# Kernel tuning notes

Measured on AMD Instinct MI355X. Metric: run time of the kernel, lower is better.

## Reference

```python
import jax, jax.numpy as jnp
import numpy as np

D = 1024
H = 16
L = 2048
B = 2
EPS = 1e-5


def setup_inputs() -> dict:
    key = jax.random.key(0)
    ks = jax.random.split(key, 12)
    s = 0.02
    return {
        "x": jax.random.normal(ks[0], (B, L, D), dtype=jnp.float32),
        "ln1_w": jnp.ones((D,), jnp.float32),
        "ln1_b": jnp.zeros((D,), jnp.float32),
        "ln2_w": jnp.ones((D,), jnp.float32),
        "ln2_b": jnp.zeros((D,), jnp.float32),
        "attn_w": jax.random.normal(ks[1], (D, 3 * D), jnp.float32) * s,
        "attn_b": jnp.zeros((3 * D,), jnp.float32),
        "proj_w": jax.random.normal(ks[2], (D, D), jnp.float32) * s,
        "proj_b": jnp.zeros((D,), jnp.float32),
        "fc1_w": jax.random.normal(ks[3], (D, 4 * D), jnp.float32) * s,
        "fc1_b": jnp.zeros((4 * D,), jnp.float32),
        "fc2_w": jax.random.normal(ks[4], (4 * D, D), jnp.float32) * s,
        "fc2_b": jnp.zeros((D,), jnp.float32),
    }


def layernorm(x, w, b):
    mu = jnp.mean(x, axis=-1, keepdims=True)
    var = jnp.mean(jnp.square(x - mu), axis=-1, keepdims=True)
    return (x - mu) * jax.lax.rsqrt(var + EPS) * w + b


def reference(x, ln1_w, ln1_b, ln2_w, ln2_b, attn_w, attn_b,
              proj_w, proj_b, fc1_w, fc1_b, fc2_w, fc2_b):
    Bsz, Lq, C = x.shape
    hd = C // H

    # --- attention branch ---
    h = layernorm(x, ln1_w, ln1_b)
    qkv = h @ attn_w + attn_b                      # [B, L, 3C]
    q, k, v = jnp.split(qkv, 3, axis=-1)
    q = q.reshape(Bsz, Lq, H, hd).transpose(0, 2, 1, 3)  # [B, H, L, hd]
    k = k.reshape(Bsz, Lq, H, hd).transpose(0, 2, 1, 3)
    v = v.reshape(Bsz, Lq, H, hd).transpose(0, 2, 1, 3)

    # NOTE: original scales by 1/sqrt(embedding_dim), not sqrt(head_dim)
    att = jnp.einsum('bhqd,bhkd->bhqk', q, k) / jnp.sqrt(jnp.float32(C))
    causal = jnp.tril(jnp.ones((Lq, Lq), dtype=bool))
    att = jnp.where(causal[None, None], att, jnp.float32(-jnp.inf))
    att = jax.nn.softmax(att, axis=-1)
    y = jnp.einsum('bhqk,bhkd->bhqd', att, v)      # [B, H, L, hd]
    y = y.transpose(0, 2, 1, 3).reshape(Bsz, Lq, C)
    y = y @ proj_w + proj_b
    x = x + y

    # --- MLP branch ---
    h = layernorm(x, ln2_w, ln2_b)
    h = jax.nn.gelu(h @ fc1_w + fc1_b, approximate=False)
    h = h @ fc2_w + fc2_b
    return x + h
```

## Files before the change

### kernel.cpp

```cpp
#include <hip/hip_runtime.h>

#define Bsz 2
#define Lq  2048
#define Dm  1024
#define Hh  16

typedef __attribute__((ext_vector_type(8))) short bf16x8;
typedef __attribute__((ext_vector_type(4))) float f32x4;

#define MFMA16(a, b, c) __builtin_amdgcn_mfma_f32_16x16x32_bf16((a), (b), (c), 0, 0, 0)
#define EXP2F(x) __builtin_amdgcn_exp2f(x)

__device__ __forceinline__ short f2bf(float f) {
    union { float f; unsigned u; } v; v.f = f;
    unsigned r = v.u + 0x7fffu + ((v.u >> 16) & 1u);
    return (short)(r >> 16);
}

__device__ __forceinline__ float bf2f(unsigned short s) {
    union { float f; unsigned u; } t; t.u = ((unsigned)s) << 16;
    return t.f;
}

__device__ __forceinline__ int pk2(float a, float b) {
    union { float f; unsigned u; } ua, ub; ua.f = a; ub.f = b;
    return (int)((ua.u >> 16) | (ub.u & 0xffff0000u));
}

__device__ __forceinline__ void gload16(const void* g, void* l) {
    __builtin_amdgcn_global_load_lds((const __attribute__((address_space(1))) void*)g,
                                     (__attribute__((address_space(3))) void*)l,
                                     16, 0, 0);
}

__global__ __launch_bounds__(256) void ln_bf16(const float* __restrict__ x,
                                               const float* __restrict__ w,
                                               const float* __restrict__ b,
                                               short* __restrict__ out) {
    const int row = blockIdx.x;
    const int tid = threadIdx.x;
    const float4 v = ((const float4*)(x + (size_t)row * 1024))[tid];
    float s = v.x + v.y + v.z + v.w;
    float q = v.x * v.x + v.y * v.y + v.z * v.z + v.w * v.w;
    for (int off = 32; off > 0; off >>= 1) {
        s += __shfl_down(s, off);
        q += __shfl_down(q, off);
    }
    __shared__ float red[8];
    const int wave = tid >> 6;
    if ((tid & 63) == 0) { red[wave] = s; red[wave + 4] = q; }
    __syncthreads();
    s = red[0] + red[1] + red[2] + red[3];
    q = red[4] + red[5] + red[6] + red[7];
    const float mu = s * (1.0f / 1024.0f);
    const float var = q * (1.0f / 1024.0f) - mu * mu;
    const float rstd = rsqrtf(var + 1e-5f);
    const float4 wv = ((const float4*)w)[tid];
    const float4 bv = ((const float4*)b)[tid];
    short4 o;
    o.x = f2bf((v.x - mu) * rstd * wv.x + bv.x);
    o.y = f2bf((v.y - mu) * rstd * wv.y + bv.y);
    o.z = f2bf((v.z - mu) * rstd * wv.z + bv.z);
    o.w = f2bf((v.w - mu) * rstd * wv.w + bv.w);
    ((short4*)(out + (size_t)row * 1024))[tid] = o;
}

__global__ __launch_bounds__(256) void tr_cvt_all(
    const float* __restrict__ attnw, const float* __restrict__ projw,
    const float* __restrict__ fc1w,  const float* __restrict__ fc2w,
    short* __restrict__ attnwT, short* __restrict__ projwT,
    short* __restrict__ fc1wT,  short* __restrict__ fc2wT) {
    int id = blockIdx.x;
    const float* W; short* Wt; int K, N, bx, by;
    if (id < 3072)      { W = attnw; Wt = attnwT; K = 1024; N = 3072; bx = id % 96;  by = id / 96; }
    else if (id < 4096) { id -= 3072; W = projw; Wt = projwT; K = 1024; N = 1024; bx = id & 31; by = id >> 5; }
    else if (id < 8192) { id -= 4096; W = fc1w;  Wt = fc1wT;  K = 1024; N = 4096; bx = id & 127; by = id >> 7; }
    else                { id -= 8192; W = fc2w;  Wt = fc2wT;  K = 4096; N = 1024; bx = id & 31; by = id >> 5; }
    __shared__ float t[32][33];
    const int n0 = bx * 32, k0 = by * 32;
    const int tx = threadIdx.x & 31, ty = threadIdx.x >> 5;
#pragma unroll
    for (int i = 0; i < 4; i++)
        t[ty + i * 8][tx] = W[(size_t)(k0 + ty + i * 8) * N + n0 + tx];
    __syncthreads();
#pragma unroll
    for (int i = 0; i < 4; i++)
        Wt[(size_t)(n0 + ty + i * 8) * K + k0 + tx] = f2bf(t[tx][ty + i * 8]);
}

template <int EP>
__global__ __launch_bounds__(256, 4) void gemm_bt(
    const short* __restrict__ A, const short* __restrict__ Bt,
    const float* __restrict__ bias, int N, int K,
    short* __restrict__ qd, short* __restrict__ kd, short* __restrict__ vtd,
    short* __restrict__ outb) {
    __shared__ short As[128 * 32];
    __shared__ short Bs[128 * 32];
    const int tid = threadIdx.x;
    const int lane = tid & 63, w = tid >> 6;
    const int l16 = lane & 15, quad = lane >> 4;
    const int wr = (w & 1) * 64, wc = (w >> 1) * 64;
    const int n = blockIdx.x;
    const int row0 = ((n & 7) * 4 + ((n >> 3) & 3)) * 128;
    const int col0 = (n >> 5) * 128;
    const int srow = lane >> 2, scol = (lane & 3) * 8;

    f32x4 acc[4][4];
    const f32x4 z = {0.f, 0.f, 0.f, 0.f};
#pragma unroll
    for (int i = 0; i < 4; i++)
#pragma unroll
        for (int j = 0; j < 4; j++) acc[i][j] = z;

    const size_t arow = (size_t)(row0 + w * 32 + srow);
    const size_t brow = (size_t)(col0 + w * 32 + srow);

    for (int k0 = 0; k0 < K; k0 += 32) {
        gload16(A + arow * K + k0 + scol,        &As[(w * 32) * 32]);
        gload16(A + (arow + 16) * K + k0 + scol, &As[(w * 32 + 16) * 32]);
        gload16(Bt + brow * K + k0 + scol,        &Bs[(w * 32) * 32]);
        gload16(Bt + (brow + 16) * K + k0 + scol, &Bs[(w * 32 + 16) * 32]);
        __syncthreads();
        bf16x8 a[4], bb[4];
#pragma unroll
        for (int i = 0; i < 4; i++) a[i] = *(const bf16x8*)&As[(wr + i * 16 + l16) * 32 + quad * 8];
#pragma unroll
        for (int j = 0; j < 4; j++) bb[j] = *(const bf16x8*)&Bs[(wc + j * 16 + l16) * 32 + quad * 8];
#pragma unroll
        for (int i = 0; i < 4; i++)
#pragma unroll
            for (int j = 0; j < 4; j++) acc[i][j] = MFMA16(a[i], bb[j], acc[i][j]);
        __syncthreads();
    }

    float bz[4];
#pragma unroll
    for (int j = 0; j < 4; j++) bz[j] = bias[col0 + wc + j * 16 + l16];

#pragma unroll
    for (int i = 0; i < 4; i++) {
#pragma unroll
        for (int r = 0; r < 4; r++) {
            const int grow = row0 + wr + i * 16 + quad * 4 + r;
#pragma unroll
            for (int j = 0; j < 4; j++) {
                const int gcol = col0 + wc + j * 16 + l16;
                const float v = acc[i][j][r] + bz[j];
                if constexpr (EP == 0) {
                    const int b = grow >> 11, l = grow & 2047;
                    const int sec = gcol >> 10, wi = gcol & 1023;
                    const int h = wi >> 6, d = wi & 63;
                    if (sec == 2) {
                        vtd[(((size_t)b * Hh + h) * 64 + d) * Lq + l] = f2bf(v);
                    } else {
                        short* dst = sec ? kd : qd;
                        dst[(((size_t)b * Hh + h) * Lq + l) * 64 + d] = f2bf(v);
                    }
                } else {
                    const float g = 0.5f * v * (1.0f + erff(v * 0.70710678118f));
                    outb[(size_t)grow * N + gcol] = f2bf(g);
                }
            }
        }
    }
}

__global__ __launch_bounds__(256, 4) void gemm_sk(
    const short* __restrict__ A, const short* __restrict__ Bt, int K, int zbits,
    short* __restrict__ Cp) {
    __shared__ short As[128 * 32];
    __shared__ short Bs[128 * 32];
    const int tid = threadIdx.x;
    const int lane = tid & 63, w = tid >> 6;
    const int l16 = lane & 15, quad = lane >> 4;
    const int wr = (w & 1) * 64, wc = (w >> 1) * 64;
    const int n = blockIdx.x;
    const int xcd = n & 7, t = n >> 3;
    const int col = t & 7, u = t >> 3;
    const int c = xcd * (4 << zbits) + u;
    const int zsl = c & ((1 << zbits) - 1);
    const int row0 = (c >> zbits) * 128, col0 = col * 128;
    const int KS = K >> zbits;
    const int kbeg = zsl * KS, kend = kbeg + KS;
    const int srow = lane >> 2, scol = (lane & 3) * 8;

    f32x4 acc[4][4];
    const f32x4 z = {0.f, 0.f, 0.f, 0.f};
#pragma unroll
    for (int i = 0; i < 4; i++)
#pragma unroll
        for (int j = 0; j < 4; j++) acc[i][j] = z;

    const size_t arow = (size_t)(row0 + w * 32 + srow);
    const size_t brow = (size_t)(col0 + w * 32 + srow);

    for (int k0 = kbeg; k0 < kend; k0 += 32) {
        gload16(A + arow * K + k0 + scol,        &As[(w * 32) * 32]);
        gload16(A + (arow + 16) * K + k0 + scol, &As[(w * 32 + 16) * 32]);
        gload16(Bt + brow * K + k0 + scol,        &Bs[(w * 32) * 32]);
        gload16(Bt + (brow + 16) * K + k0 + scol, &Bs[(w * 32 + 16) * 32]);
        __syncthreads();
        bf16x8 a[4], bb[4];
#pragma unroll
        for (int i = 0; i < 4; i++) a[i] = *(const bf16x8*)&As[(wr + i * 16 + l16) * 32 + quad * 8];
#pragma unroll
        for (int j = 0; j < 4; j++) bb[j] = *(const bf16x8*)&Bs[(wc + j * 16 + l16) * 32 + quad * 8];
#pragma unroll
        for (int i = 0; i < 4; i++)
#pragma unroll
            for (int j = 0; j < 4; j++) acc[i][j] = MFMA16(a[i], bb[j], acc[i][j]);
        __syncthreads();
    }

    short* cp = Cp + (size_t)zsl * 4096 * 1024;
#pragma unroll
    for (int i = 0; i < 4; i++) {
#pragma unroll
        for (int r = 0; r < 4; r++) {
            const int grow = row0 + wr + i * 16 + quad * 4 + r;
#pragma unroll
            for (int j = 0; j < 4; j++) {
                const int gcol = col0 + wc + j * 16 + l16;
                cp[(size_t)grow * 1024 + gcol] = f2bf(acc[i][j][r]);
            }
        }
    }
}

__global__ __launch_bounds__(256) void sk_reduce(const short* __restrict__ Cp, int S,
                                                 const float* __restrict__ res,
                                                 const float* __restrict__ bias,
                                                 float* __restrict__ out) {
    const int row = blockIdx.x, tid = threadIdx.x;
    const size_t base = (size_t)row * 1024 + tid * 4;
    float4 a = ((const float4*)(res + (size_t)row * 1024))[tid];
    const float4 bz = ((const float4*)bias)[tid];
    a.x += bz.x; a.y += bz.y; a.z += bz.z; a.w += bz.w;
    for (int s = 0; s < S; s++) {
        const ushort4 c = *(const ushort4*)(Cp + (size_t)s * 4096 * 1024 + base);
        a.x += bf2f(c.x); a.y += bf2f(c.y); a.z += bf2f(c.z); a.w += bf2f(c.w);
    }
    *(float4*)(out + base) = a;
}

__global__ __launch_bounds__(256) void sk_reduce_ln(const short* __restrict__ Cp, int S,
                                                    const float* __restrict__ res,
                                                    const float* __restrict__ bias,
                                                    const float* __restrict__ lnw,
                                                    const float* __restrict__ lnb,
                                                    float* __restrict__ xout,
                                                    short* __restrict__ hout) {
    const int row = blockIdx.x, tid = threadIdx.x;
    const size_t base = (size_t)row * 1024 + tid * 4;
    float4 a = ((const float4*)(res + (size_t)row * 1024))[tid];
    const float4 bz = ((const float4*)bias)[tid];
    a.x += bz.x; a.y += bz.y; a.z += bz.z; a.w += bz.w;
    for (int s = 0; s < S; s++) {
        const ushort4 c = *(const ushort4*)(Cp + (size_t)s * 4096 * 1024 + base);
        a.x += bf2f(c.x); a.y += bf2f(c.y); a.z += bf2f(c.z); a.w += bf2f(c.w);
    }
    *(float4*)(xout + base) = a;
    float sm = a.x + a.y + a.z + a.w;
    float qs = a.x * a.x + a.y * a.y + a.z * a.z + a.w * a.w;
    for (int off = 32; off > 0; off >>= 1) {
        sm += __shfl_down(sm, off);
        qs += __shfl_down(qs, off);
    }
    __shared__ float red[8];
    const int wave = tid >> 6;
    if ((tid & 63) == 0) { red[wave] = sm; red[wave + 4] = qs; }
    __syncthreads();
    sm = red[0] + red[1] + red[2] + red[3];
    qs = red[4] + red[5] + red[6] + red[7];
    const float mu = sm * (1.0f / 1024.0f);
    const float var = qs * (1.0f / 1024.0f) - mu * mu;
    const float rstd = rsqrtf(var + 1e-5f);
    const float4 wv = ((const float4*)lnw)[tid];
    const float4 bv = ((const float4*)lnb)[tid];
    short4 o;
    o.x = f2bf((a.x - mu) * rstd * wv.x + bv.x);
    o.y = f2bf((a.y - mu) * rstd * wv.y + bv.y);
    o.z = f2bf((a.z - mu) * rstd * wv.z + bv.z);
    o.w = f2bf((a.w - mu) * rstd * wv.w + bv.w);
    ((short4*)(hout + (size_t)row * 1024))[tid] = o;
}

#define KP 72
__global__ __launch_bounds__(256, 2) void attn_kernel(const short* __restrict__ Q,
                                                      const short* __restrict__ Kb,
                                                      const short* __restrict__ Vt,
                                                      short* __restrict__ Y) {
    const int tid = threadIdx.x;
    const int lane = tid & 63, wave = tid >> 6;
    const int l16 = lane & 15, quad = lane >> 4;
    const int qblk = 15 - blockIdx.x;
    const int bh = blockIdx.y;
    const int qw = qblk * 128 + wave * 32;

    const short* qg = Q + ((size_t)bh * Lq + qw) * 64;
    const short* kg = Kb + (size_t)bh * Lq * 64;
    const short* vg = Vt + (size_t)bh * 64 * Lq;

    __shared__ short sKa[2][64 * 32], sKb[2][64 * 32];
    __shared__ short sVa[2][64 * 32], sVb[2][64 * 32];
    __shared__ short sP[4][32 * KP];
    short* wpP = sP[wave];

    const float c1 = 0.0450842213f;

    bf16x8 qf[2][2];
#pragma unroll
    for (int c = 0; c < 2; c++)
#pragma unroll
        for (int d = 0; d < 2; d++) {
            bf16x8 v = *(const bf16x8*)(qg + (c * 16 + l16) * 64 + d * 32 + quad * 8);
            bf16x8 r;
#pragma unroll
            for (int i = 0; i < 8; i++) {
                union { float f; unsigned u; } t;
                t.u = ((unsigned)(unsigned short)v[i]) << 16;
                r[i] = f2bf(t.f * c1);
            }
            qf[c][d] = r;
        }

    f32x4 o[4][2];
    const f32x4 z = {0.f, 0.f, 0.f, 0.f};
#pragma unroll
    for (int j = 0; j < 4; j++)
#pragma unroll
        for (int c = 0; c < 2; c++) o[j][c] = z;
    float l_i[2] = {0.f, 0.f};

    const int srow = wave * 16 + (lane >> 2);
    const int scol = (lane & 3) * 8;
    const int nst = 2 * qblk + 2;

    auto stage = [&](int s) {
        const int p = s & 1;
        const int kb = s * 64;
        gload16(kg + (size_t)(kb + srow) * 64 + scol,      &sKa[p][(wave * 16) * 32]);
        gload16(kg + (size_t)(kb + srow) * 64 + 32 + scol, &sKb[p][(wave * 16) * 32]);
        gload16(vg + (size_t)srow * Lq + kb + scol,        &sVa[p][(wave * 16) * 32]);
        gload16(vg + (size_t)srow * Lq + kb + 32 + scol,   &sVb[p][(wave * 16) * 32]);
    };

    stage(0);

    for (int s = 0; s < nst; ++s) {
        const int p = s & 1;
        __syncthreads();
        bf16x8 kf[4][2];
#pragma unroll
        for (int kt = 0; kt < 4; kt++) {
            kf[kt][0] = *(const bf16x8*)&sKa[p][(kt * 16 + l16) * 32 + quad * 8];
            kf[kt][1] = *(const bf16x8*)&sKb[p][(kt * 16 + l16) * 32 + quad * 8];
        }
        if (s + 1 < nst) stage(s + 1);

        f32x4 st[4][2];
#pragma unroll
        for (int kt = 0; kt < 4; kt++)
#pragma unroll
            for (int c = 0; c < 2; c++) {
                st[kt][c] = MFMA16(kf[kt][0], qf[c][0], z);
                st[kt][c] = MFMA16(kf[kt][1], qf[c][1], st[kt][c]);
            }

        const int rel = s * 64 - qblk * 128 - wave * 32;
        if (rel > -64) {
#pragma unroll
            for (int kt = 0; kt < 4; kt++)
#pragma unroll
                for (int c = 0; c < 2; c++)
#pragma unroll
                    for (int r = 0; r < 4; r++) {
                        const int krel = rel + kt * 16 + quad * 4 + r - c * 16;
                        if (krel > l16) st[kt][c][r] = -1e30f;
                    }
        }

#pragma unroll
        for (int c = 0; c < 2; c++) {
            float pv[4][4], rs = 0.f;
#pragma unroll
            for (int kt = 0; kt < 4; kt++)
#pragma unroll
                for (int r = 0; r < 4; r++) {
                    pv[kt][r] = EXP2F(st[kt][c][r]);
                    rs += pv[kt][r];
                }
            l_i[c] += rs;
            short* wp = wpP + (c * 16 + l16) * KP;
#pragma unroll
            for (int kt = 0; kt < 4; kt++) {
                int2 pw; pw.x = pk2(pv[kt][0], pv[kt][1]); pw.y = pk2(pv[kt][2], pv[kt][3]);
                *(int2*)(wp + kt * 16 + quad * 4) = pw;
            }
        }

        bf16x8 pf[2][2];
#pragma unroll
        for (int c = 0; c < 2; c++) {
            pf[c][0] = *(const bf16x8*)(wpP + (c * 16 + l16) * KP + quad * 8);
            pf[c][1] = *(const bf16x8*)(wpP + (c * 16 + l16) * KP + 32 + quad * 8);
        }
#pragma unroll
        for (int j = 0; j < 4; j++) {
            const bf16x8 v0 = *(const bf16x8*)&sVa[p][(j * 16 + l16) * 32 + quad * 8];
            const bf16x8 v1 = *(const bf16x8*)&sVb[p][(j * 16 + l16) * 32 + quad * 8];
#pragma unroll
            for (int c = 0; c < 2; c++) {
                o[j][c] = MFMA16(v0, pf[c][0], o[j][c]);
                o[j][c] = MFMA16(v1, pf[c][1], o[j][c]);
            }
        }
    }

    const int b = bh >> 4, h = bh & 15;
#pragma unroll
    for (int c = 0; c < 2; c++) {
        float ls = l_i[c];
        ls += __shfl_xor(ls, 16);
        ls += __shfl_xor(ls, 32);
        const float inv = 1.0f / ls;
        const size_t base = ((size_t)b * Lq + qw + c * 16 + l16) * 1024 + h * 64;
#pragma unroll
        for (int j = 0; j < 4; j++) {
            short4 s4;
            s4.x = f2bf(o[j][c][0] * inv);
            s4.y = f2bf(o[j][c][1] * inv);
            s4.z = f2bf(o[j][c][2] * inv);
            s4.w = f2bf(o[j][c][3] * inv);
            *(short4*)(Y + base + j * 16 + quad * 4) = s4;
        }
    }
}

extern "C" void kernel_launch(void* const* d_in, const int* in_sizes, int n_in,
                              void* d_out, int out_size, void* d_ws, size_t ws_size,
                              hipStream_t stream) {
    (void)in_sizes; (void)n_in; (void)out_size; (void)ws_size;
    const float* x     = (const float*)d_in[0];
    const float* ln1w  = (const float*)d_in[1];
    const float* ln1b  = (const float*)d_in[2];
    const float* ln2w  = (const float*)d_in[3];
    const float* ln2b  = (const float*)d_in[4];
    const float* attnw = (const float*)d_in[5];
    const float* attnb = (const float*)d_in[6];
    const float* projw = (const float*)d_in[7];
    const float* projb = (const float*)d_in[8];
    const float* fc1w  = (const float*)d_in[9];
    const float* fc1b  = (const float*)d_in[10];
    const float* fc2w  = (const float*)d_in[11];
    const float* fc2b  = (const float*)d_in[12];
    float* out = (float*)d_out;

    char* ws = (char*)d_ws;
    size_t off = 0;
    auto alloc = [&](size_t bytes) {
        void* p = ws + off;
        off += (bytes + 255) & ~(size_t)255;
        return p;
    };
    short* attnwT = (short*)alloc(3072ull * 1024 * 2);
    short* projwT = (short*)alloc(1024ull * 1024 * 2);
    short* fc1wT  = (short*)alloc(4096ull * 1024 * 2);
    short* fc2wT  = (short*)alloc(1024ull * 4096 * 2);
    short* hbuf   = (short*)alloc(4096ull * 1024 * 2);
    short* qbuf   = (short*)alloc(4096ull * 1024 * 2);
    short* kbuf   = (short*)alloc(4096ull * 1024 * 2);
    short* vtbuf  = (short*)alloc(4096ull * 1024 * 2);
    short* ybuf   = (short*)alloc(4096ull * 1024 * 2);
    float* x1     = (float*)alloc(4096ull * 1024 * 4);
    short* Cp     = (short*)alloc(4ull * 4096 * 1024 * 2);
    short* hh = qbuf;

    tr_cvt_all<<<12288, 256, 0, stream>>>(attnw, projw, fc1w, fc2w,
                                          attnwT, projwT, fc1wT, fc2wT);

    ln_bf16<<<4096, 256, 0, stream>>>(x, ln1w, ln1b, hbuf);
    gemm_bt<0><<<768, 256, 0, stream>>>(hbuf, attnwT, attnb, 3072, 1024,
                                        qbuf, kbuf, vtbuf, nullptr);
    attn_kernel<<<dim3(16, 32), 256, 0, stream>>>(qbuf, kbuf, vtbuf, ybuf);
    gemm_sk<<<512, 256, 0, stream>>>(ybuf, projwT, 1024, 1, Cp);
    sk_reduce_ln<<<4096, 256, 0, stream>>>(Cp, 2, x, projb, ln2w, ln2b, x1, hbuf);

    gemm_bt<2><<<1024, 256, 0, stream>>>(hbuf, fc1wT, fc1b, 4096, 1024,
                                         nullptr, nullptr, nullptr, hh);
    gemm_sk<<<1024, 256, 0, stream>>>(hh, fc2wT, 4096, 2, Cp);
    sk_reduce<<<4096, 256, 0, stream>>>(Cp, 4, x1, fc2b, out);
}
```

Baseline: 341.9 us.

## Replace GEMMs with 256x256-tile, 4-stage pipelined, LDS-swizzled kernel

```diff
diff --git a/kernel.cpp b/kernel.cpp
--- a/kernel.cpp
+++ b/kernel.cpp
@@ -89,64 +89,105 @@
 }
 
 template <int EP>
-__global__ __launch_bounds__(256, 4) void gemm_bt(
+__global__ __launch_bounds__(512, 2) void gemm256(
     const short* __restrict__ A, const short* __restrict__ Bt,
-    const float* __restrict__ bias, int N, int K,
+    const float* __restrict__ bias, int N, int K, int zbits,
     short* __restrict__ qd, short* __restrict__ kd, short* __restrict__ vtd,
     short* __restrict__ outb) {
-    __shared__ short As[128 * 32];
-    __shared__ short Bs[128 * 32];
+    __shared__ short sA[4][8192];
+    __shared__ short sB[4][8192];
     const int tid = threadIdx.x;
     const int lane = tid & 63, w = tid >> 6;
     const int l16 = lane & 15, quad = lane >> 4;
-    const int wr = (w & 1) * 64, wc = (w >> 1) * 64;
-    const int n = blockIdx.x;
-    const int row0 = ((n & 7) * 4 + ((n >> 3) & 3)) * 128;
-    const int col0 = (n >> 5) * 128;
-    const int srow = lane >> 2, scol = (lane & 3) * 8;
-
-    f32x4 acc[4][4];
+    const int wm = w >> 2, wn = w & 3;
+
+    const int wg = (blockIdx.x & 7) * ((int)gridDim.x >> 3) + ((int)blockIdx.x >> 3);
+    const int bm = wg & 15, rest = wg >> 4;
+    int bn, zsl = 0, kbase = 0, klen = K;
+    if constexpr (EP == 3) {
+        bn = rest & 3; zsl = rest >> 2;
+        klen = K >> zbits; kbase = zsl * klen;
+    } else {
+        bn = rest;
+    }
+    const int row0 = bm << 8, col0 = bn << 8;
+    const int NT = klen >> 5;
+
+    const int srow = w * 16 + (lane >> 2);
+    const int sslot = (lane & 3) ^ ((lane >> 2) & 3) ^ (lane >> 4);
+    const short* gA = A + (size_t)(row0 + srow) * K + kbase + sslot * 8;
+    const short* gB = Bt + (size_t)(col0 + srow) * K + kbase + sslot * 8;
+    const size_t rstr = (size_t)128 * K;
+
+    auto stage = [&](int t) {
+        const int p = t & 3;
+        const int ko = t << 5;
+        short* la = &sA[p][(w * 16) * 32];
+        short* lb = &sB[p][(w * 16) * 32];
+        gload16(gA + ko, la);
+        gload16(gA + rstr + ko, la + 4096);
+        gload16(gB + ko, lb);
+        gload16(gB + rstr + ko, lb + 4096);
+    };
+
+    f32x4 acc[8][4];
     const f32x4 z = {0.f, 0.f, 0.f, 0.f};
 #pragma unroll
-    for (int i = 0; i < 4; i++)
-#pragma unroll
-        for (int j = 0; j < 4; j++) acc[i][j] = z;
-
-    const size_t arow = (size_t)(row0 + w * 32 + srow);
-    const size_t brow = (size_t)(col0 + w * 32 + srow);
-
-    for (int k0 = 0; k0 < K; k0 += 32) {
-        gload16(A + arow * K + k0 + scol,        &As[(w * 32) * 32]);
-        gload16(A + (arow + 16) * K + k0 + scol, &As[(w * 32 + 16) * 32]);
-        gload16(Bt + brow * K + k0 + scol,        &Bs[(w * 32) * 32]);
-        gload16(Bt + (brow + 16) * K + k0 + scol, &Bs[(w * 32 + 16) * 32]);
-        __syncthreads();
-        bf16x8 a[4], bb[4];
-#pragma unroll
-        for (int i = 0; i < 4; i++) a[i] = *(const bf16x8*)&As[(wr + i * 16 + l16) * 32 + quad * 8];
-#pragma unroll
-        for (int j = 0; j < 4; j++) bb[j] = *(const bf16x8*)&Bs[(wc + j * 16 + l16) * 32 + quad * 8];
-#pragma unroll
-        for (int i = 0; i < 4; i++)
-#pragma unroll
-            for (int j = 0; j < 4; j++) acc[i][j] = MFMA16(a[i], bb[j], acc[i][j]);
-        __syncthreads();
+    for (int m = 0; m < 8; m++)
+#pragma unroll
+        for (int j = 0; j < 4; j++) acc[m][j] = z;
+
+    stage(0); stage(1); stage(2);
+
+    const int rslot = quad ^ (l16 & 3) ^ (l16 >> 2);
+    const int aoff = (wm * 128 + l16) * 32 + rslot * 8;
+    const int boff = (wn * 64 + l16) * 32 + rslot * 8;
+
+    for (int t = 0; t < NT; ++t) {
+        if (t + 3 < NT) stage(t + 3);
+        const int rem = NT - 1 - t;
+        if (rem >= 3)      asm volatile("s_waitcnt vmcnt(12)" ::: "memory");
+        else if (rem == 2) asm volatile("s_waitcnt vmcnt(8)" ::: "memory");
+        else if (rem == 1) asm volatile("s_waitcnt vmcnt(4)" ::: "memory");
+        else               asm volatile("s_waitcnt vmcnt(0)" ::: "memory");
+        __builtin_amdgcn_s_barrier();
+        __builtin_amdgcn_sched_barrier(0);
+        const int p = t & 3;
+        bf16x8 af[8], bf[4];
+#pragma unroll
+        for (int m = 0; m < 8; m++) af[m] = *(const bf16x8*)&sA[p][aoff + m * 512];
+#pragma unroll
+        for (int j = 0; j < 4; j++) bf[j] = *(const bf16x8*)&sB[p][boff + j * 512];
+        __builtin_amdgcn_s_setprio(1);
+#pragma unroll
+        for (int m = 0; m < 8; m++)
+#pragma unroll
+            for (int j = 0; j < 4; j++) acc[m][j] = MFMA16(af[m], bf[j], acc[m][j]);
+        __builtin_amdgcn_s_setprio(0);
+        asm volatile("s_waitcnt lgkmcnt(0)" ::: "memory");
+        __builtin_amdgcn_sched_barrier(0);
+        __builtin_amdgcn_s_barrier();
+        __builtin_amdgcn_sched_barrier(0);
     }
 
     float bz[4];
-#pragma unroll
-    for (int j = 0; j < 4; j++) bz[j] = bias[col0 + wc + j * 16 + l16];
-
-#pragma unroll
-    for (int i = 0; i < 4; i++) {
+    if constexpr (EP != 3) {
+#pragma unroll
+        for (int j = 0; j < 4; j++) bz[j] = bias[col0 + wn * 64 + j * 16 + l16];
+    }
+    short* cp = nullptr;
+    if constexpr (EP == 3) cp = outb + (size_t)zsl * 4096 * 1024;
+
+#pragma unroll
+    for (int m = 0; m < 8; m++) {
 #pragma unroll
         for (int r = 0; r < 4; r++) {
-            const int grow = row0 + wr + i * 16 + quad * 4 + r;
+            const int grow = row0 + wm * 128 + m * 16 + quad * 4 + r;
 #pragma unroll
             for (int j = 0; j < 4; j++) {
-                const int gcol = col0 + wc + j * 16 + l16;
-                const float v = acc[i][j][r] + bz[j];
+                const int gcol = col0 + wn * 64 + j * 16 + l16;
                 if constexpr (EP == 0) {
+                    const float v = acc[m][j][r] + bz[j];
                     const int b = grow >> 11, l = grow & 2047;
                     const int sec = gcol >> 10, wi = gcol & 1023;
                     const int h = wi >> 6, d = wi & 63;
@@ -156,72 +197,13 @@
                         short* dst = sec ? kd : qd;
                         dst[(((size_t)b * Hh + h) * Lq + l) * 64 + d] = f2bf(v);
                     }
-                } else {
+                } else if constexpr (EP == 2) {
+                    const float v = acc[m][j][r] + bz[j];
                     const float g = 0.5f * v * (1.0f + erff(v * 0.70710678118f));
                     outb[(size_t)grow * N + gcol] = f2bf(g);
+                } else {
+                    cp[(size_t)grow * 1024 + gcol] = f2bf(acc[m][j][r]);
                 }
-            }
-        }
-    }
-}
-
-__global__ __launch_bounds__(256, 4) void gemm_sk(
-    const short* __restrict__ A, const short* __restrict__ Bt, int K, int zbits,
-    short* __restrict__ Cp) {
-    __shared__ short As[128 * 32];
-    __shared__ short Bs[128 * 32];
-    const int tid = threadIdx.x;
-    const int lane = tid & 63, w = tid >> 6;
-    const int l16 = lane & 15, quad = lane >> 4;
-    const int wr = (w & 1) * 64, wc = (w >> 1) * 64;
-    const int n = blockIdx.x;
-    const int xcd = n & 7, t = n >> 3;
-    const int col = t & 7, u = t >> 3;
-    const int c = xcd * (4 << zbits) + u;
-    const int zsl = c & ((1 << zbits) - 1);
-    const int row0 = (c >> zbits) * 128, col0 = col * 128;
-    const int KS = K >> zbits;
-    const int kbeg = zsl * KS, kend = kbeg + KS;
-    const int srow = lane >> 2, scol = (lane & 3) * 8;
-
-    f32x4 acc[4][4];
-    const f32x4 z = {0.f, 0.f, 0.f, 0.f};
-#pragma unroll
-    for (int i = 0; i < 4; i++)
-#pragma unroll
-        for (int j = 0; j < 4; j++) acc[i][j] = z;
-
-    const size_t arow = (size_t)(row0 + w * 32 + srow);
-    const size_t brow = (size_t)(col0 + w * 32 + srow);
-
-    for (int k0 = kbeg; k0 < kend; k0 += 32) {
-        gload16(A + arow * K + k0 + scol,        &As[(w * 32) * 32]);
-        gload16(A + (arow + 16) * K + k0 + scol, &As[(w * 32 + 16) * 32]);
-        gload16(Bt + brow * K + k0 + scol,        &Bs[(w * 32) * 32]);
-        gload16(Bt + (brow + 16) * K + k0 + scol, &Bs[(w * 32 + 16) * 32]);
-        __syncthreads();
-        bf16x8 a[4], bb[4];
-#pragma unroll
-        for (int i = 0; i < 4; i++) a[i] = *(const bf16x8*)&As[(wr + i * 16 + l16) * 32 + quad * 8];
-#pragma unroll
-        for (int j = 0; j < 4; j++) bb[j] = *(const bf16x8*)&Bs[(wc + j * 16 + l16) * 32 + quad * 8];
-#pragma unroll
-        for (int i = 0; i < 4; i++)
-#pragma unroll
-            for (int j = 0; j < 4; j++) acc[i][j] = MFMA16(a[i], bb[j], acc[i][j]);
-        __syncthreads();
-    }
-
-    short* cp = Cp + (size_t)zsl * 4096 * 1024;
-#pragma unroll
-    for (int i = 0; i < 4; i++) {
-#pragma unroll
-        for (int r = 0; r < 4; r++) {
-            const int grow = row0 + wr + i * 16 + quad * 4 + r;
-#pragma unroll
-            for (int j = 0; j < 4; j++) {
-                const int gcol = col0 + wc + j * 16 + l16;
-                cp[(size_t)grow * 1024 + gcol] = f2bf(acc[i][j][r]);
             }
         }
     }
@@ -480,14 +462,16 @@
                                           attnwT, projwT, fc1wT, fc2wT);
 
     ln_bf16<<<4096, 256, 0, stream>>>(x, ln1w, ln1b, hbuf);
-    gemm_bt<0><<<768, 256, 0, stream>>>(hbuf, attnwT, attnb, 3072, 1024,
+    gemm256<0><<<192, 512, 0, stream>>>(hbuf, attnwT, attnb, 3072, 1024, 0,
                                         qbuf, kbuf, vtbuf, nullptr);
     attn_kernel<<<dim3(16, 32), 256, 0, stream>>>(qbuf, kbuf, vtbuf, ybuf);
-    gemm_sk<<<512, 256, 0, stream>>>(ybuf, projwT, 1024, 1, Cp);
+    gemm256<3><<<128, 512, 0, stream>>>(ybuf, projwT, nullptr, 1024, 1024, 1,
+                                        nullptr, nullptr, nullptr, Cp);
     sk_reduce_ln<<<4096, 256, 0, stream>>>(Cp, 2, x, projb, ln2w, ln2b, x1, hbuf);
 
-    gemm_bt<2><<<1024, 256, 0, stream>>>(hbuf, fc1wT, fc1b, 4096, 1024,
-                                         nullptr, nullptr, nullptr, hh);
-    gemm_sk<<<1024, 256, 0, stream>>>(hh, fc2wT, 4096, 2, Cp);
+    gemm256<2><<<256, 512, 0, stream>>>(hbuf, fc1wT, fc1b, 4096, 1024, 0,
+                                        nullptr, nullptr, nullptr, hh);
+    gemm256<3><<<256, 512, 0, stream>>>(hh, fc2wT, nullptr, 1024, 4096, 2,
+                                        nullptr, nullptr, nullptr, Cp);
     sk_reduce<<<4096, 256, 0, stream>>>(Cp, 4, x1, fc2b, out);
 }
```

New measurement: 407.2 us. 1.19x slower.

## Double GEMM K-tile to 64 with XOR-swizzled shared-memory layout

Applied to the files above, without the earlier changes.

```diff
diff --git a/kernel.cpp b/kernel.cpp
--- a/kernel.cpp
+++ b/kernel.cpp
@@ -94,8 +94,8 @@
     const float* __restrict__ bias, int N, int K,
     short* __restrict__ qd, short* __restrict__ kd, short* __restrict__ vtd,
     short* __restrict__ outb) {
-    __shared__ short As[128 * 32];
-    __shared__ short Bs[128 * 32];
+    __shared__ short As[128 * 64];
+    __shared__ short Bs[128 * 64];
     const int tid = threadIdx.x;
     const int lane = tid & 63, w = tid >> 6;
     const int l16 = lane & 15, quad = lane >> 4;
@@ -103,7 +103,8 @@
     const int n = blockIdx.x;
     const int row0 = ((n & 7) * 4 + ((n >> 3) & 3)) * 128;
     const int col0 = (n >> 5) * 128;
-    const int srow = lane >> 2, scol = (lane & 3) * 8;
+    const int srow = lane >> 3;
+    const int scol = ((lane & 7) ^ srow) * 8;
 
     f32x4 acc[4][4];
     const f32x4 z = {0.f, 0.f, 0.f, 0.f};
@@ -115,21 +116,26 @@
     const size_t arow = (size_t)(row0 + w * 32 + srow);
     const size_t brow = (size_t)(col0 + w * 32 + srow);
 
-    for (int k0 = 0; k0 < K; k0 += 32) {
-        gload16(A + arow * K + k0 + scol,        &As[(w * 32) * 32]);
-        gload16(A + (arow + 16) * K + k0 + scol, &As[(w * 32 + 16) * 32]);
-        gload16(Bt + brow * K + k0 + scol,        &Bs[(w * 32) * 32]);
-        gload16(Bt + (brow + 16) * K + k0 + scol, &Bs[(w * 32 + 16) * 32]);
+    for (int k0 = 0; k0 < K; k0 += 64) {
+#pragma unroll
+        for (int g = 0; g < 4; g++) {
+            gload16(A + (arow + g * 8) * K + k0 + scol,  &As[(w * 32 + g * 8) * 64]);
+            gload16(Bt + (brow + g * 8) * K + k0 + scol, &Bs[(w * 32 + g * 8) * 64]);
+        }
         __syncthreads();
-        bf16x8 a[4], bb[4];
-#pragma unroll
-        for (int i = 0; i < 4; i++) a[i] = *(const bf16x8*)&As[(wr + i * 16 + l16) * 32 + quad * 8];
-#pragma unroll
-        for (int j = 0; j < 4; j++) bb[j] = *(const bf16x8*)&Bs[(wc + j * 16 + l16) * 32 + quad * 8];
-#pragma unroll
-        for (int i = 0; i < 4; i++)
-#pragma unroll
-            for (int j = 0; j < 4; j++) acc[i][j] = MFMA16(a[i], bb[j], acc[i][j]);
+#pragma unroll
+        for (int kk = 0; kk < 2; kk++) {
+            const int rsl = ((kk * 4 + quad) ^ (l16 & 7)) * 8;
+            bf16x8 a[4], bb[4];
+#pragma unroll
+            for (int i = 0; i < 4; i++) a[i] = *(const bf16x8*)&As[(wr + i * 16 + l16) * 64 + rsl];
+#pragma unroll
+            for (int j = 0; j < 4; j++) bb[j] = *(const bf16x8*)&Bs[(wc + j * 16 + l16) * 64 + rsl];
+#pragma unroll
+            for (int i = 0; i < 4; i++)
+#pragma unroll
+                for (int j = 0; j < 4; j++) acc[i][j] = MFMA16(a[i], bb[j], acc[i][j]);
+        }
         __syncthreads();
     }
 
@@ -168,8 +174,8 @@
 __global__ __launch_bounds__(256, 4) void gemm_sk(
     const short* __restrict__ A, const short* __restrict__ Bt, int K, int zbits,
     short* __restrict__ Cp) {
-    __shared__ short As[128 * 32];
-    __shared__ short Bs[128 * 32];
+    __shared__ short As[128 * 64];
+    __shared__ short Bs[128 * 64];
     const int tid = threadIdx.x;
     const int lane = tid & 63, w = tid >> 6;
     const int l16 = lane & 15, quad = lane >> 4;
@@ -182,7 +188,8 @@
     const int row0 = (c >> zbits) * 128, col0 = col * 128;
     const int KS = K >> zbits;
     const int kbeg = zsl * KS, kend = kbeg + KS;
-    const int srow = lane >> 2, scol = (lane & 3) * 8;
+    const int srow = lane >> 3;
+    const int scol = ((lane & 7) ^ srow) * 8;
 
     f32x4 acc[4][4];
     const f32x4 z = {0.f, 0.f, 0.f, 0.f};
@@ -194,21 +201,26 @@
     const size_t arow = (size_t)(row0 + w * 32 + srow);
     const size_t brow = (size_t)(col0 + w * 32 + srow);
 
-    for (int k0 = kbeg; k0 < kend; k0 += 32) {
-        gload16(A + arow * K + k0 + scol,        &As[(w * 32) * 32]);
-        gload16(A + (arow + 16) * K + k0 + scol, &As[(w * 32 + 16) * 32]);
-        gload16(Bt + brow * K + k0 + scol,        &Bs[(w * 32) * 32]);
-        gload16(Bt + (brow + 16) * K + k0 + scol, &Bs[(w * 32 + 16) * 32]);
+    for (int k0 = kbeg; k0 < kend; k0 += 64) {
+#pragma unroll
+        for (int g = 0; g < 4; g++) {
+            gload16(A + (arow + g * 8) * K + k0 + scol,  &As[(w * 32 + g * 8) * 64]);
+            gload16(Bt + (brow + g * 8) * K + k0 + scol, &Bs[(w * 32 + g * 8) * 64]);
+        }
         __syncthreads();
-        bf16x8 a[4], bb[4];
-#pragma unroll
-        for (int i = 0; i < 4; i++) a[i] = *(const bf16x8*)&As[(wr + i * 16 + l16) * 32 + quad * 8];
-#pragma unroll
-        for (int j = 0; j < 4; j++) bb[j] = *(const bf16x8*)&Bs[(wc + j * 16 + l16) * 32 + quad * 8];
-#pragma unroll
-        for (int i = 0; i < 4; i++)
-#pragma unroll
-            for (int j = 0; j < 4; j++) acc[i][j] = MFMA16(a[i], bb[j], acc[i][j]);
+#pragma unroll
+        for (int kk = 0; kk < 2; kk++) {
+            const int rsl = ((kk * 4 + quad) ^ (l16 & 7)) * 8;
+            bf16x8 a[4], bb[4];
+#pragma unroll
+            for (int i = 0; i < 4; i++) a[i] = *(const bf16x8*)&As[(wr + i * 16 + l16) * 64 + rsl];
+#pragma unroll
+            for (int j = 0; j < 4; j++) bb[j] = *(const bf16x8*)&Bs[(wc + j * 16 + l16) * 64 + rsl];
+#pragma unroll
+            for (int i = 0; i < 4; i++)
+#pragma unroll
+                for (int j = 0; j < 4; j++) acc[i][j] = MFMA16(a[i], bb[j], acc[i][j]);
+        }
         __syncthreads();
     }
 
```

After: 340.6 us. Within noise of the previous version (-0.4%).
